# Kernel tuning notes

Measured on AMD Instinct MI355X. Metric: run time of the kernel, lower is better.

Reference implementation:

```python
import jax, jax.numpy as jnp
import numpy as np

N, M, DIM_K, DIM_V = 8192, 8192, 256, 256

def setup_inputs() -> dict:
    key = jax.random.key(0)
    kq, kk, kv = jax.random.split(key, 3)
    Q = jax.random.normal(kq, (N, DIM_K), dtype=jnp.float32)
    K = jax.random.normal(kk, (M, DIM_K), dtype=jnp.float32)
    V = jax.random.normal(kv, (M, DIM_V), dtype=jnp.float32)
    return {"Q": Q, "K": K, "V": V}

def reference(Q, K, V):
    # scores: [N, M] = Q @ K^T / sqrt(dim_k)
    scale = 1.0 / jnp.sqrt(jnp.asarray(Q.shape[-1], dtype=Q.dtype))
    scores = jnp.einsum('nd,md->nm', Q, K) * scale
    attn = jax.nn.softmax(scores, axis=-1)  # softmax over keys
    return attn @ V  # [N, dim_v]
```

## Files before the change

### kernel.cpp

```cpp
#include <hip/hip_runtime.h>
#include <hip/hip_bf16.h>
#include <hip/hip_fp16.h>


typedef __attribute__((ext_vector_type(16))) float floatx16;
typedef __attribute__((ext_vector_type(8)))  short short8;

union S8u { short8 v; unsigned short u[8]; };

#if __has_builtin(__builtin_amdgcn_exp2f)
#define EXP2F(x) __builtin_amdgcn_exp2f(x)
#else
#define EXP2F(x) exp2f(x)
#endif

__device__ __forceinline__ unsigned short f2bf(float f) {
    unsigned int u = __builtin_bit_cast(unsigned int, f);
    unsigned int r = u + 0x7fffu + ((u >> 16) & 1u);
    return (unsigned short)(r >> 16);
}

__device__ __forceinline__ unsigned cvtpk_bf16(float lo, float hi) {
    unsigned r;
    asm("v_cvt_pk_bf16_f32 %0, %1, %2" : "=v"(r) : "v"(lo), "v"(hi));
    return r;
}

__device__ __forceinline__ void gload16(const void* g, void* l) {
    __builtin_amdgcn_global_load_lds(
        (const __attribute__((address_space(1))) unsigned int*)g,
        (__attribute__((address_space(3))) unsigned int*)l, 16, 0, 0);
}


__global__ void cvt_bf16_kernel(const float* __restrict__ in,
                                unsigned short* __restrict__ out,
                                float scale, int n8) {
    int i = blockIdx.x * blockDim.x + threadIdx.x;
    if (i >= n8) return;
    const float4* p = reinterpret_cast<const float4*>(in) + (size_t)i * 2;
    float4 a = p[0], b = p[1];
    S8u r;
    r.u[0] = f2bf(a.x * scale); r.u[1] = f2bf(a.y * scale);
    r.u[2] = f2bf(a.z * scale); r.u[3] = f2bf(a.w * scale);
    r.u[4] = f2bf(b.x * scale); r.u[5] = f2bf(b.y * scale);
    r.u[6] = f2bf(b.z * scale); r.u[7] = f2bf(b.w * scale);
    *reinterpret_cast<short8*>(out + (size_t)i * 8) = r.v;
}

__global__ void transpose_v_kernel(const float* __restrict__ V,
                                   unsigned short* __restrict__ Vt) {
    __shared__ unsigned short T[64][72];
    const int kv0 = blockIdx.x * 64;
    const int v0  = blockIdx.y * 64;
    const int tid = threadIdx.x;
#pragma unroll
    for (int it = 0; it < 4; ++it) {
        int flat = it * 256 + tid;
        int r  = flat >> 4;
        int c4 = (flat & 15) * 4;
        float4 f = *reinterpret_cast<const float4*>(
            V + (size_t)(kv0 + r) * 256 + v0 + c4);
        T[c4 + 0][r] = f2bf(f.x);
        T[c4 + 1][r] = f2bf(f.y);
        T[c4 + 2][r] = f2bf(f.z);
        T[c4 + 3][r] = f2bf(f.w);
    }
    __syncthreads();
#pragma unroll
    for (int it = 0; it < 2; ++it) {
        int flat = it * 256 + tid;
        int r  = flat >> 3;
        int c8 = (flat & 7) * 8;
        short8 v8 = *reinterpret_cast<const short8*>(&T[r][c8]);
        *reinterpret_cast<short8*>(Vt + (size_t)(v0 + r) * 8192 + kv0 + c8) = v8;
    }
}


#define MFMA_B16 __builtin_amdgcn_mfma_f32_32x32x16_bf16

__global__ __launch_bounds__(256, 2)
void attn_kernel(const float* __restrict__ Qf,
                 const unsigned short* __restrict__ Kb,
                 const unsigned short* __restrict__ VtG,
                 __half* __restrict__ Opart,
                 float* __restrict__ Ml,
                 int kv_span, int gshift) {
    __shared__ __align__(16) unsigned char lds[2][32768];

    const int tid  = threadIdx.x;
    const int lane = tid & 63;
    const int w    = tid >> 6;
    const int l31  = lane & 31;
    const int h    = lane >> 5;

    const int ngm1 = (1 << gshift) - 1;
    const int id   = blockIdx.x + 64 * blockIdx.y;
    const int g    = id & ngm1;
    const int qblk = id >> gshift;
    const int kv_begin = g * kv_span;
    const int tiles = kv_span >> 5;
    const int q0 = qblk * 128 + w * 32;

    const float qs = 0.09016844005556021f;
    short8 qf[16];
    {
        const float* qp = Qf + (size_t)(q0 + l31) * 256 + h * 8;
#pragma unroll
        for (int ds = 0; ds < 16; ++ds) {
            float4 f0 = *reinterpret_cast<const float4*>(qp + ds * 16);
            float4 f1 = *reinterpret_cast<const float4*>(qp + ds * 16 + 4);
            uint4 uu;
            uu.x = cvtpk_bf16(f0.x * qs, f0.y * qs);
            uu.y = cvtpk_bf16(f0.z * qs, f0.w * qs);
            uu.z = cvtpk_bf16(f1.x * qs, f1.y * qs);
            uu.w = cvtpk_bf16(f1.z * qs, f1.w * qs);
            qf[ds] = __builtin_bit_cast(short8, uu);
        }
    }

    floatx16 o[8];
#pragma unroll
    for (int vt = 0; vt < 8; ++vt)
#pragma unroll
        for (int r = 0; r < 16; ++r) o[vt][r] = 0.f;
    float m_run = -1e30f, l_run = 0.f;

    int offk[4], offv[4];
#pragma unroll
    for (int i = 0; i < 4; ++i) {
        int j  = i * 256 + tid;
        int rk = j >> 5, ck = (j & 31) ^ (rk & 7);
        offk[i] = rk * 256 + ck * 8;
        int rv = j >> 2, cv = (j & 3) ^ ((rv >> 1) & 3);
        offv[i] = rv * 8192 + cv * 8;
    }

    auto STAGE = [&](int kv0, int bufsel) {
        unsigned char* kb = &lds[bufsel][0];
        unsigned char* vb = &lds[bufsel][16384];
        const unsigned short* ks = Kb + (size_t)kv0 * 256;
        const unsigned short* vs = VtG + kv0;
#pragma unroll
        for (int i = 0; i < 4; ++i) {
            int base = (i * 256 + w * 64) * 16;
            gload16(ks + offk[i], kb + base);
            gload16(vs + offv[i], vb + base);
        }
    };

    STAGE(kv_begin, 0);
    asm volatile("s_waitcnt vmcnt(0)" ::: "memory");
    __syncthreads();

    const int swz  = l31 & 7;
    const int vswz = (l31 >> 1) & 3;

    auto buildPA = [&](const floatx16& sv, int rbase) -> short8 {
        unsigned cpk0 = cvtpk_bf16(sv[rbase + 0], sv[rbase + 1]);
        unsigned cpk1 = cvtpk_bf16(sv[rbase + 2], sv[rbase + 3]);
        unsigned cpk2 = cvtpk_bf16(sv[rbase + 4], sv[rbase + 5]);
        unsigned cpk3 = cvtpk_bf16(sv[rbase + 6], sv[rbase + 7]);
        uint4 uu;
#if __has_builtin(__builtin_amdgcn_permlane32_swap)
        auto r02 = __builtin_amdgcn_permlane32_swap((int)cpk0, (int)cpk2, false, false);
        auto r13 = __builtin_amdgcn_permlane32_swap((int)cpk1, (int)cpk3, false, false);
        uu.x = (unsigned)r02[0]; uu.y = (unsigned)r13[0];
        uu.z = (unsigned)r02[1]; uu.w = (unsigned)r13[1];
#else
        unsigned send0 = h ? cpk0 : cpk2;
        unsigned send1 = h ? cpk1 : cpk3;
        unsigned r0 = (unsigned)__shfl_xor((int)send0, 32);
        unsigned r1 = (unsigned)__shfl_xor((int)send1, 32);
        uu.x = h ? r0 : cpk0;
        uu.y = h ? r1 : cpk1;
        uu.z = h ? cpk2 : r0;
        uu.w = h ? cpk3 : r1;
#endif
        return __builtin_bit_cast(short8, uu);
    };

    for (int t = 0; t < tiles; ++t) {
        const int cur = t & 1;
        if (t + 1 < tiles) STAGE(kv_begin + (t + 1) * 32, cur ^ 1);

        const unsigned char* kl = &lds[cur][0];
        const unsigned char* vl = &lds[cur][16384];

        floatx16 s0;
#pragma unroll
        for (int r = 0; r < 16; ++r) s0[r] = 0.f;
        __builtin_amdgcn_s_setprio(1);
#pragma unroll
        for (int ds = 0; ds < 16; ++ds) {
            int c0 = (ds * 2 + h) ^ swz;
            short8 a0 = *reinterpret_cast<const short8*>(
                kl + (size_t)l31 * 512 + c0 * 16);
            s0 = MFMA_B16(a0, qf[ds], s0, 0, 0, 0);
        }
        __builtin_amdgcn_s_setprio(0);

        {
            float t4[4];
#pragma unroll
            for (int i = 0; i < 4; ++i)
                t4[i] = fmaxf(fmaxf(s0[i], s0[i + 4]),
                              fmaxf(s0[i + 8], s0[i + 12]));
            float mt = fmaxf(fmaxf(t4[0], t4[1]), fmaxf(t4[2], t4[3]));
            mt = fmaxf(mt, __shfl_xor(mt, 32));
            if (__any(mt > m_run + 11.5f)) {
                float mnew = fmaxf(m_run, mt);
                float al = EXP2F(m_run - mnew);
                m_run = mnew;
                l_run *= al;
#pragma unroll
                for (int reg = 0; reg < 16; ++reg) {
                    int srcl = ((reg & 3) + 8 * (reg >> 2)) + 4 * h;
                    float alr = __shfl(al, srcl);
#pragma unroll
                    for (int vt = 0; vt < 8; ++vt) o[vt][reg] *= alr;
                }
            }
#pragma unroll
            for (int r = 0; r < 16; ++r) s0[r] = EXP2F(s0[r] - m_run);
            float u[4];
#pragma unroll
            for (int i = 0; i < 4; ++i)
                u[i] = (s0[i] + s0[i + 4]) + (s0[i + 8] + s0[i + 12]);
            float lt = (u[0] + u[1]) + (u[2] + u[3]);
            lt += __shfl_xor(lt, 32);
            l_run += lt;
        }

        __builtin_amdgcn_s_setprio(1);
#pragma unroll
        for (int kk = 0; kk < 2; ++kk) {
            short8 pa = buildPA(s0, kk * 8);
            int cvs = (kk * 2 + h) ^ vswz;
#pragma unroll
            for (int vt = 0; vt < 8; ++vt) {
                short8 b = *reinterpret_cast<const short8*>(
                    vl + (size_t)(vt * 32 + l31) * 64 + cvs * 16);
                o[vt] = MFMA_B16(pa, b, o[vt], 0, 0, 0);
            }
        }
        __builtin_amdgcn_s_setprio(0);

        asm volatile("s_waitcnt vmcnt(0)" ::: "memory");
        __syncthreads();
    }

    const size_t gq = (size_t)g * 8192;
    float linv = 1.0f / l_run;
#pragma unroll
    for (int reg = 0; reg < 16; ++reg) {
        int row = (reg & 3) + 8 * (reg >> 2) + 4 * h;
        float li = __shfl(linv, row);
#pragma unroll
        for (int vt = 0; vt < 8; ++vt)
            Opart[(gq + q0 + row) * 256 + vt * 32 + l31] =
                __float2half_rn(o[vt][reg] * li);
    }
    if (h == 0) {
        size_t idx = (gq + q0 + l31) * 2;
        Ml[idx]     = m_run;
        Ml[idx + 1] = l_run;
    }
}


__global__ void merge_kernel(const __half* __restrict__ Opart,
                             const float* __restrict__ Ml,
                             float* __restrict__ out, int ngroups) {
    int row = blockIdx.x;
    int col = threadIdx.x;
    float m = -1e30f;
    for (int g = 0; g < ngroups; ++g)
        m = fmaxf(m, Ml[((size_t)g * 8192 + row) * 2]);
    float den = 0.f, acc = 0.f;
    for (int g = 0; g < ngroups; ++g) {
        float wg = EXP2F(Ml[((size_t)g * 8192 + row) * 2] - m) *
                   Ml[((size_t)g * 8192 + row) * 2 + 1];
        den += wg;
        acc += wg * __half2float(Opart[((size_t)g * 8192 + row) * 256 + col]);
    }
    out[(size_t)row * 256 + col] = acc / den;
}


extern "C" void kernel_launch(void* const* d_in, const int* in_sizes, int n_in,
                              void* d_out, int out_size, void* d_ws, size_t ws_size,
                              hipStream_t stream) {
    const float* Q = (const float*)d_in[0];
    const float* K = (const float*)d_in[1];
    const float* V = (const float*)d_in[2];
    float* out = (float*)d_out;

    unsigned short* Kb = (unsigned short*)d_ws;
    unsigned short* Vt = Kb + (size_t)8192 * 256;

    const size_t base = (size_t)8192 * 256 * 2 * 2;
    const size_t osz  = (size_t)8192 * 256 * 2;
    const size_t mlsz = (size_t)8192 * 2 * 4;

    int gshift = 3;
    for (; gshift > 0; --gshift)
        if (base + ((osz + mlsz) << gshift) <= ws_size) break;
    int ng = 1 << gshift;

    __half* Opart = (__half*)((char*)d_ws + base);
    float*  Mlp   = (float*)((char*)d_ws + base + osz * (size_t)ng);

    const int n8 = 8192 * 256 / 8;
    cvt_bf16_kernel<<<n8 / 256, 256, 0, stream>>>(K, Kb, 1.0f, n8);
    transpose_v_kernel<<<dim3(128, 4), 256, 0, stream>>>(V, Vt);
    attn_kernel<<<dim3(64, ng), 256, 0, stream>>>(Q, Kb, Vt, Opart, Mlp,
                                                  8192 / ng, gshift);
    merge_kernel<<<8192, 256, 0, stream>>>(Opart, Mlp, out, ng);
}
```

Baseline: 131.9 us.

## Split attention into producer QK/softmax warps and consumer PV warps

The attention block grows from 256 to 512 threads. Four producer waves compute QK^T scores and the softmax, then write the bf16 probabilities, rescale factors and flags into LDS. Four consumer waves hold the output accumulators and run the P·V MFMAs one tile behind, so score and PV work can overlap across waves, and K and V staging are split and offset. The cost is more LDS traffic for P, an extra tile of latency, and higher LDS use with 512 threads and launch_bounds(512,2), which may limit occupancy.

```diff
diff --git a/kernel.cpp b/kernel.cpp
--- a/kernel.cpp
+++ b/kernel.cpp
@@ -80,20 +80,27 @@
 
 #define MFMA_B16 __builtin_amdgcn_mfma_f32_32x32x16_bf16
 
-__global__ __launch_bounds__(256, 2)
+__global__ __launch_bounds__(512, 2)
 void attn_kernel(const float* __restrict__ Qf,
                  const unsigned short* __restrict__ Kb,
                  const unsigned short* __restrict__ VtG,
                  __half* __restrict__ Opart,
                  float* __restrict__ Ml,
                  int kv_span, int gshift) {
-    __shared__ __align__(16) unsigned char lds[2][32768];
+    __shared__ __align__(16) unsigned char kbuf[2][16384];
+    __shared__ __align__(16) unsigned char vbuf[2][16384];
+    __shared__ __align__(16) unsigned char pbuf[2][4][2048];
+    __shared__ float albuf[2][4][32];
+    __shared__ float flagbuf[2][4];
+    __shared__ float lfin[4][32];
 
     const int tid  = threadIdx.x;
     const int lane = tid & 63;
     const int w    = tid >> 6;
     const int l31  = lane & 31;
     const int h    = lane >> 5;
+    const int qt   = w & 3;
+    const bool prod = (w < 4);
 
     const int ngm1 = (1 << gshift) - 1;
     const int id   = blockIdx.x + 64 * blockIdx.y;
@@ -101,11 +108,11 @@
     const int qblk = id >> gshift;
     const int kv_begin = g * kv_span;
     const int tiles = kv_span >> 5;
-    const int q0 = qblk * 128 + w * 32;
+    const int q0 = qblk * 128 + qt * 32;
 
     const float qs = 0.09016844005556021f;
     short8 qf[16];
-    {
+    if (prod) {
         const float* qp = Qf + (size_t)(q0 + l31) * 256 + h * 8;
 #pragma unroll
         for (int ds = 0; ds < 16; ++ds) {
@@ -119,42 +126,44 @@
             qf[ds] = __builtin_bit_cast(short8, uu);
         }
     }
-
     floatx16 o[8];
-#pragma unroll
-    for (int vt = 0; vt < 8; ++vt)
-#pragma unroll
-        for (int r = 0; r < 16; ++r) o[vt][r] = 0.f;
+    if (!prod) {
+#pragma unroll
+        for (int vt = 0; vt < 8; ++vt)
+#pragma unroll
+            for (int r = 0; r < 16; ++r) o[vt][r] = 0.f;
+    }
     float m_run = -1e30f, l_run = 0.f;
 
-    int offk[4], offv[4];
-#pragma unroll
-    for (int i = 0; i < 4; ++i) {
-        int j  = i * 256 + tid;
+    int offk[2], offv[2];
+#pragma unroll
+    for (int i = 0; i < 2; ++i) {
+        int j  = i * 512 + tid;
         int rk = j >> 5, ck = (j & 31) ^ (rk & 7);
         offk[i] = rk * 256 + ck * 8;
         int rv = j >> 2, cv = (j & 3) ^ ((rv >> 1) & 3);
         offv[i] = rv * 8192 + cv * 8;
     }
 
-    auto STAGE = [&](int kv0, int bufsel) {
-        unsigned char* kb = &lds[bufsel][0];
-        unsigned char* vb = &lds[bufsel][16384];
+    auto STAGEK = [&](int kv0, int bufsel) {
         const unsigned short* ks = Kb + (size_t)kv0 * 256;
+#pragma unroll
+        for (int i = 0; i < 2; ++i)
+            gload16(ks + offk[i], &kbuf[bufsel][(i * 512 + w * 64) * 16]);
+    };
+    auto STAGEV = [&](int kv0, int bufsel) {
         const unsigned short* vs = VtG + kv0;
 #pragma unroll
-        for (int i = 0; i < 4; ++i) {
-            int base = (i * 256 + w * 64) * 16;
-            gload16(ks + offk[i], kb + base);
-            gload16(vs + offv[i], vb + base);
-        }
+        for (int i = 0; i < 2; ++i)
+            gload16(vs + offv[i], &vbuf[bufsel][(i * 512 + w * 64) * 16]);
     };
 
-    STAGE(kv_begin, 0);
+    STAGEK(kv_begin, 0);
     asm volatile("s_waitcnt vmcnt(0)" ::: "memory");
     __syncthreads();
 
     const int swz  = l31 & 7;
+    const int pswz = l31 & 3;
     const int vswz = (l31 >> 1) & 3;
 
     auto buildPA = [&](const floatx16& sv, int rbase) -> short8 {
@@ -181,91 +190,124 @@
         return __builtin_bit_cast(short8, uu);
     };
 
-    for (int t = 0; t < tiles; ++t) {
-        const int cur = t & 1;
-        if (t + 1 < tiles) STAGE(kv_begin + (t + 1) * 32, cur ^ 1);
-
-        const unsigned char* kl = &lds[cur][0];
-        const unsigned char* vl = &lds[cur][16384];
-
-        floatx16 s0;
-#pragma unroll
-        for (int r = 0; r < 16; ++r) s0[r] = 0.f;
-        __builtin_amdgcn_s_setprio(1);
-#pragma unroll
-        for (int ds = 0; ds < 16; ++ds) {
-            int c0 = (ds * 2 + h) ^ swz;
-            short8 a0 = *reinterpret_cast<const short8*>(
-                kl + (size_t)l31 * 512 + c0 * 16);
-            s0 = MFMA_B16(a0, qf[ds], s0, 0, 0, 0);
-        }
-        __builtin_amdgcn_s_setprio(0);
-
-        {
-            float t4[4];
-#pragma unroll
-            for (int i = 0; i < 4; ++i)
-                t4[i] = fmaxf(fmaxf(s0[i], s0[i + 4]),
-                              fmaxf(s0[i + 8], s0[i + 12]));
-            float mt = fmaxf(fmaxf(t4[0], t4[1]), fmaxf(t4[2], t4[3]));
-            mt = fmaxf(mt, __shfl_xor(mt, 32));
-            if (__any(mt > m_run + 11.5f)) {
-                float mnew = fmaxf(m_run, mt);
-                float al = EXP2F(m_run - mnew);
-                m_run = mnew;
-                l_run *= al;
+    for (int i = 0; i <= tiles; ++i) {
+        if (i + 1 < tiles) STAGEK(kv_begin + (i + 1) * 32, (i + 1) & 1);
+        if (i < tiles)     STAGEV(kv_begin + i * 32, i & 1);
+
+        if (prod && i < tiles) {
+            const unsigned char* kl = kbuf[i & 1];
+            floatx16 sA, sB;
+#pragma unroll
+            for (int r = 0; r < 16; ++r) { sA[r] = 0.f; sB[r] = 0.f; }
+            __builtin_amdgcn_s_setprio(1);
+#pragma unroll
+            for (int ds = 0; ds < 8; ++ds) {
+                int c0 = (ds * 2 + h) ^ swz;
+                short8 a0 = *reinterpret_cast<const short8*>(
+                    kl + (size_t)l31 * 512 + c0 * 16);
+                sA = MFMA_B16(a0, qf[ds], sA, 0, 0, 0);
+            }
+#pragma unroll
+            for (int ds = 8; ds < 16; ++ds) {
+                int c0 = (ds * 2 + h) ^ swz;
+                short8 a0 = *reinterpret_cast<const short8*>(
+                    kl + (size_t)l31 * 512 + c0 * 16);
+                sB = MFMA_B16(a0, qf[ds], sB, 0, 0, 0);
+            }
+            __builtin_amdgcn_s_setprio(0);
+            floatx16 s0;
+#pragma unroll
+            for (int r = 0; r < 16; ++r) s0[r] = sA[r] + sB[r];
+
+            float alv = 1.0f; float flg = 0.0f;
+            {
+                float t4[4];
+#pragma unroll
+                for (int k = 0; k < 4; ++k)
+                    t4[k] = fmaxf(fmaxf(s0[k], s0[k + 4]),
+                                  fmaxf(s0[k + 8], s0[k + 12]));
+                float mt = fmaxf(fmaxf(t4[0], t4[1]), fmaxf(t4[2], t4[3]));
+                mt = fmaxf(mt, __shfl_xor(mt, 32));
+                if (__any(mt > m_run + 11.5f)) {
+                    float mnew = fmaxf(m_run, mt);
+                    alv = EXP2F(m_run - mnew);
+                    m_run = mnew;
+                    l_run *= alv;
+                    flg = 1.0f;
+                }
+#pragma unroll
+                for (int r = 0; r < 16; ++r) s0[r] = EXP2F(s0[r] - m_run);
+                float u[4];
+#pragma unroll
+                for (int k = 0; k < 4; ++k)
+                    u[k] = (s0[k] + s0[k + 4]) + (s0[k + 8] + s0[k + 12]);
+                float lt = (u[0] + u[1]) + (u[2] + u[3]);
+                lt += __shfl_xor(lt, 32);
+                l_run += lt;
+            }
+#pragma unroll
+            for (int kk = 0; kk < 2; ++kk) {
+                short8 pa = buildPA(s0, kk * 8);
+                *reinterpret_cast<short8*>(
+                    &pbuf[i & 1][qt][l31 * 64 + (((kk * 2 + h) ^ pswz) * 16)]) = pa;
+            }
+            if (h == 0) albuf[i & 1][qt][l31] = alv;
+            if (lane == 0) flagbuf[i & 1][qt] = flg;
+        }
+
+        if (!prod && i >= 1) {
+            const int pb = (i - 1) & 1;
+            const unsigned char* vl = vbuf[pb];
+            float flg = flagbuf[pb][qt];
+            if (flg != 0.0f) {
 #pragma unroll
                 for (int reg = 0; reg < 16; ++reg) {
-                    int srcl = ((reg & 3) + 8 * (reg >> 2)) + 4 * h;
-                    float alr = __shfl(al, srcl);
+                    int row = (reg & 3) + 8 * (reg >> 2) + 4 * h;
+                    float alr = albuf[pb][qt][row];
 #pragma unroll
                     for (int vt = 0; vt < 8; ++vt) o[vt][reg] *= alr;
                 }
             }
-#pragma unroll
-            for (int r = 0; r < 16; ++r) s0[r] = EXP2F(s0[r] - m_run);
-            float u[4];
-#pragma unroll
-            for (int i = 0; i < 4; ++i)
-                u[i] = (s0[i] + s0[i + 4]) + (s0[i + 8] + s0[i + 12]);
-            float lt = (u[0] + u[1]) + (u[2] + u[3]);
-            lt += __shfl_xor(lt, 32);
-            l_run += lt;
-        }
-
-        __builtin_amdgcn_s_setprio(1);
-#pragma unroll
-        for (int kk = 0; kk < 2; ++kk) {
-            short8 pa = buildPA(s0, kk * 8);
-            int cvs = (kk * 2 + h) ^ vswz;
-#pragma unroll
-            for (int vt = 0; vt < 8; ++vt) {
-                short8 b = *reinterpret_cast<const short8*>(
-                    vl + (size_t)(vt * 32 + l31) * 64 + cvs * 16);
-                o[vt] = MFMA_B16(pa, b, o[vt], 0, 0, 0);
-            }
-        }
-        __builtin_amdgcn_s_setprio(0);
+            __builtin_amdgcn_s_setprio(1);
+#pragma unroll
+            for (int kk = 0; kk < 2; ++kk) {
+                short8 pa = *reinterpret_cast<const short8*>(
+                    &pbuf[pb][qt][l31 * 64 + (((kk * 2 + h) ^ pswz) * 16)]);
+                int cvs = (kk * 2 + h) ^ vswz;
+#pragma unroll
+                for (int vt = 0; vt < 8; ++vt) {
+                    short8 b = *reinterpret_cast<const short8*>(
+                        vl + (size_t)(vt * 32 + l31) * 64 + cvs * 16);
+                    o[vt] = MFMA_B16(pa, b, o[vt], 0, 0, 0);
+                }
+            }
+            __builtin_amdgcn_s_setprio(0);
+        }
 
         asm volatile("s_waitcnt vmcnt(0)" ::: "memory");
         __syncthreads();
     }
 
     const size_t gq = (size_t)g * 8192;
-    float linv = 1.0f / l_run;
-#pragma unroll
-    for (int reg = 0; reg < 16; ++reg) {
-        int row = (reg & 3) + 8 * (reg >> 2) + 4 * h;
-        float li = __shfl(linv, row);
-#pragma unroll
-        for (int vt = 0; vt < 8; ++vt)
-            Opart[(gq + q0 + row) * 256 + vt * 32 + l31] =
-                __float2half_rn(o[vt][reg] * li);
-    }
-    if (h == 0) {
-        size_t idx = (gq + q0 + l31) * 2;
-        Ml[idx]     = m_run;
-        Ml[idx + 1] = l_run;
+    if (prod) {
+        if (h == 0) {
+            lfin[qt][l31] = l_run;
+            size_t idx = (gq + q0 + l31) * 2;
+            Ml[idx]     = m_run;
+            Ml[idx + 1] = l_run;
+        }
+    }
+    __syncthreads();
+    if (!prod) {
+#pragma unroll
+        for (int reg = 0; reg < 16; ++reg) {
+            int row = (reg & 3) + 8 * (reg >> 2) + 4 * h;
+            float li = 1.0f / lfin[qt][row];
+#pragma unroll
+            for (int vt = 0; vt < 8; ++vt)
+                Opart[(gq + q0 + row) * 256 + vt * 32 + l31] =
+                    __float2half_rn(o[vt][reg] * li);
+        }
     }
 }
 
@@ -315,7 +357,7 @@
     const int n8 = 8192 * 256 / 8;
     cvt_bf16_kernel<<<n8 / 256, 256, 0, stream>>>(K, Kb, 1.0f, n8);
     transpose_v_kernel<<<dim3(128, 4), 256, 0, stream>>>(V, Vt);
-    attn_kernel<<<dim3(64, ng), 256, 0, stream>>>(Q, Kb, Vt, Opart, Mlp,
+    attn_kernel<<<dim3(64, ng), 512, 0, stream>>>(Q, Kb, Vt, Opart, Mlp,
                                                   8192 / ng, gshift);
     merge_kernel<<<8192, 256, 0, stream>>>(Opart, Mlp, out, ng);
 }
```

New measurement: 168.7 us. +27.9%, slower.

## Split K/V staging into separate pipelined loads with partial vmcnt waits

Applied to the files above, without the earlier changes.

Splits the shared double buffer into separate K and V buffers and issues the next K tile before QK^T and the next V tile after softmax. Partial vmcnt(4) waits with raw s_barrier replace full drains, so only the needed half-tile must land before each phase. It also splits the QK^T MFMA chain into two independent accumulators to shorten the dependency chain. On the last iteration it issues a redundant reload of the current tile, and correctness depends on the exact vmcnt counting and barrier placement.

```diff
diff --git a/kernel.cpp b/kernel.cpp
--- a/kernel.cpp
+++ b/kernel.cpp
@@ -87,7 +87,8 @@
                  __half* __restrict__ Opart,
                  float* __restrict__ Ml,
                  int kv_span, int gshift) {
-    __shared__ __align__(16) unsigned char lds[2][32768];
+    __shared__ __align__(16) unsigned char kbuf[2][16384];
+    __shared__ __align__(16) unsigned char vbuf[2][16384];
 
     const int tid  = threadIdx.x;
     const int lane = tid & 63;
@@ -137,22 +138,23 @@
         offv[i] = rv * 8192 + cv * 8;
     }
 
-    auto STAGE = [&](int kv0, int bufsel) {
-        unsigned char* kb = &lds[bufsel][0];
-        unsigned char* vb = &lds[bufsel][16384];
+    auto STAGEK = [&](int kv0, int bufsel) {
         const unsigned short* ks = Kb + (size_t)kv0 * 256;
+#pragma unroll
+        for (int i = 0; i < 4; ++i)
+            gload16(ks + offk[i], &kbuf[bufsel][(i * 256 + w * 64) * 16]);
+    };
+    auto STAGEV = [&](int kv0, int bufsel) {
         const unsigned short* vs = VtG + kv0;
 #pragma unroll
-        for (int i = 0; i < 4; ++i) {
-            int base = (i * 256 + w * 64) * 16;
-            gload16(ks + offk[i], kb + base);
-            gload16(vs + offv[i], vb + base);
-        }
+        for (int i = 0; i < 4; ++i)
+            gload16(vs + offv[i], &vbuf[bufsel][(i * 256 + w * 64) * 16]);
     };
 
-    STAGE(kv_begin, 0);
-    asm volatile("s_waitcnt vmcnt(0)" ::: "memory");
-    __syncthreads();
+    STAGEK(kv_begin, 0);
+    STAGEV(kv_begin, 0);
+    asm volatile("s_waitcnt vmcnt(4)" ::: "memory");
+    __builtin_amdgcn_s_barrier();
 
     const int swz  = l31 & 7;
     const int vswz = (l31 >> 1) & 3;
@@ -183,23 +185,34 @@
 
     for (int t = 0; t < tiles; ++t) {
         const int cur = t & 1;
-        if (t + 1 < tiles) STAGE(kv_begin + (t + 1) * 32, cur ^ 1);
-
-        const unsigned char* kl = &lds[cur][0];
-        const unsigned char* vl = &lds[cur][16384];
-
-        floatx16 s0;
-#pragma unroll
-        for (int r = 0; r < 16; ++r) s0[r] = 0.f;
+        const int nxt = cur ^ 1;
+        const int tn  = (t + 1 < tiles) ? t + 1 : t;
+
+        STAGEK(kv_begin + tn * 32, nxt);
+
+        const unsigned char* kl = kbuf[cur];
+        floatx16 sA, sB;
+#pragma unroll
+        for (int r = 0; r < 16; ++r) { sA[r] = 0.f; sB[r] = 0.f; }
         __builtin_amdgcn_s_setprio(1);
 #pragma unroll
-        for (int ds = 0; ds < 16; ++ds) {
+        for (int ds = 0; ds < 8; ++ds) {
             int c0 = (ds * 2 + h) ^ swz;
             short8 a0 = *reinterpret_cast<const short8*>(
                 kl + (size_t)l31 * 512 + c0 * 16);
-            s0 = MFMA_B16(a0, qf[ds], s0, 0, 0, 0);
+            sA = MFMA_B16(a0, qf[ds], sA, 0, 0, 0);
+        }
+#pragma unroll
+        for (int ds = 8; ds < 16; ++ds) {
+            int c0 = (ds * 2 + h) ^ swz;
+            short8 a0 = *reinterpret_cast<const short8*>(
+                kl + (size_t)l31 * 512 + c0 * 16);
+            sB = MFMA_B16(a0, qf[ds], sB, 0, 0, 0);
         }
         __builtin_amdgcn_s_setprio(0);
+        floatx16 s0;
+#pragma unroll
+        for (int r = 0; r < 16; ++r) s0[r] = sA[r] + sB[r];
 
         {
             float t4[4];
@@ -233,6 +246,12 @@
             l_run += lt;
         }
 
+        asm volatile("s_waitcnt vmcnt(4)" ::: "memory");
+        __builtin_amdgcn_s_barrier();
+
+        STAGEV(kv_begin + tn * 32, nxt);
+
+        const unsigned char* vl = vbuf[cur];
         __builtin_amdgcn_s_setprio(1);
 #pragma unroll
         for (int kk = 0; kk < 2; ++kk) {
@@ -247,8 +266,8 @@
         }
         __builtin_amdgcn_s_setprio(0);
 
-        asm volatile("s_waitcnt vmcnt(0)" ::: "memory");
-        __syncthreads();
+        asm volatile("s_waitcnt vmcnt(4)" ::: "memory");
+        __builtin_amdgcn_s_barrier();
     }
 
     const size_t gq = (size_t)g * 8192;
```

New measurement: 135.3 us. 1.03x slower.
